# Optimization experiments

Measured on AMD Instinct MI355X. Metric: run time of the kernel, lower is better.

The kernel has to match this reference:

```python
import jax, jax.numpy as jnp
import numpy as np
from jax import lax

B, T, E, D, A, C, FILT = 32, 1600, 1024, 1024, 512, 10, 100
SCALING = 2.0


def setup_inputs() -> dict:
    key = jax.random.key(0)
    ks = jax.random.split(key, 14)
    enc_hs_pad = jax.random.normal(ks[0], (B, T, E), dtype=jnp.float32)
    # lengths in [T//2, T] so every row has valid positions
    enc_hs_len = jax.random.randint(ks[1], (B,), T // 2, T + 1, dtype=jnp.int32)
    dec_z = jax.random.normal(ks[2], (B, D), dtype=jnp.float32)
    # previous attention weights: uniform over valid frames, normalized
    valid = (jnp.arange(T)[None, :] < enc_hs_len[:, None]).astype(jnp.float32)
    raw = jax.random.uniform(ks[3], (B, T), dtype=jnp.float32) * valid
    att_prev = raw / jnp.sum(raw, axis=1, keepdims=True)
    att_h = 0.1 * jax.random.normal(ks[4], (B, A), dtype=jnp.float32)
    att_c = 0.1 * jax.random.normal(ks[5], (B, A), dtype=jnp.float32)
    W_enc = jax.random.normal(ks[6], (A, E), dtype=jnp.float32) / np.sqrt(E)
    b_enc = jax.random.normal(ks[7], (A,), dtype=jnp.float32) * 0.01
    W_dec = jax.random.normal(ks[8], (A, D), dtype=jnp.float32) / np.sqrt(D)
    conv_w = jax.random.normal(ks[9], (C, 1, 2 * FILT + 1), dtype=jnp.float32) / np.sqrt(2 * FILT + 1)
    W_ih = jax.random.normal(ks[10], (4 * A, C), dtype=jnp.float32) / np.sqrt(C)
    W_hh = jax.random.normal(ks[11], (4 * A, A), dtype=jnp.float32) / np.sqrt(A)
    W_g = jax.random.normal(ks[12], (A,), dtype=jnp.float32) / np.sqrt(A)
    b_g = jnp.zeros((1,), dtype=jnp.float32)
    return {"enc_hs_pad": enc_hs_pad, "enc_hs_len": enc_hs_len, "dec_z": dec_z,
            "att_prev": att_prev, "att_h": att_h, "att_c": att_c,
            "W_enc": W_enc, "b_enc": b_enc, "W_dec": W_dec, "conv_w": conv_w,
            "W_ih": W_ih, "W_hh": W_hh, "W_g": W_g, "b_g": b_g}


def reference(enc_hs_pad, enc_hs_len, dec_z, att_prev, att_h, att_c,
              W_enc, b_enc, W_dec, conv_w, W_ih, W_hh, W_g, b_g):
    t_len = enc_hs_pad.shape[1]
    filts = (conv_w.shape[-1] - 1) // 2

    # precompute encoder projection (B, T, A)
    pre_enc = jnp.einsum('bte,ae->bta', enc_hs_pad, W_enc) + b_enc

    # location conv on previous attention: (B,1,T) -> (B,C,T), relu, global max-pool over T
    att_conv = lax.conv_general_dilated(att_prev[:, None, :], conv_w,
                                        window_strides=(1,), padding=[(filts, filts)],
                                        dimension_numbers=('NCH', 'OIH', 'NCH'))
    att_feat = jnp.max(jax.nn.relu(att_conv), axis=-1)  # (B, C)

    # LSTMCell (no bias), pytorch gate order i, f, g, o
    gates = att_feat @ W_ih.T + att_h @ W_hh.T  # (B, 4A)
    i, f, g, o = jnp.split(gates, 4, axis=-1)
    c_new = jax.nn.sigmoid(f) * att_c + jax.nn.sigmoid(i) * jnp.tanh(g)
    h_new = jax.nn.sigmoid(o) * jnp.tanh(c_new)  # (B, A)

    dec_proj = dec_z @ W_dec.T  # (B, A)
    # scores (B, T)
    e = jnp.tanh(h_new[:, None, :] + pre_enc + dec_proj[:, None, :]) @ W_g + b_g

    mask = jnp.arange(t_len)[None, :] >= enc_hs_len[:, None]  # True = pad
    e = jnp.where(mask, jnp.finfo(e.dtype).min, e)
    w = jax.nn.softmax(SCALING * e, axis=1)  # (B, T)

    ctx = jnp.einsum('bt,bte->be', w, enc_hs_pad)  # (B, E)
    return ctx, w, h_new, c_new
```

## Files before the change

kernel.cpp:

```cpp
#include <hip/hip_runtime.h>
#include <hip/hip_bf16.h>

#define BB 32
#define TT 1600
#define EE 1024
#define AA 512
#define CC 10
#define KW 201

typedef __attribute__((ext_vector_type(8))) short short8;
typedef __attribute__((ext_vector_type(4))) float f32x4;

__device__ __forceinline__ float sigm(float x) { return 1.f / (1.f + expf(-x)); }

__device__ __forceinline__ unsigned int cvt2(float a, float b) {
    float2 f2; f2.x = a; f2.y = b;
    __hip_bfloat162 h = __float22bfloat162_rn(f2);
    unsigned int r;
    __builtin_memcpy(&r, &h, 4);
    return r;
}

__device__ __forceinline__ void gl_lds16(const void* g, void* l) {
    __builtin_amdgcn_global_load_lds(
        (const __attribute__((address_space(1))) unsigned int*)g,
        (__attribute__((address_space(3))) unsigned int*)l, 16, 0, 0);
}

#define AF_OFF   0
#define R_OFF    320
#define E_OFF    16704
#define WBF_OFF  67904

#define CTX_OFF 0
#define W_OFF   32768
#define H_OFF   83968
#define C_OFF   100352

__global__ void prep_kernel(const float* __restrict__ att_prev,
                            const float* __restrict__ conv_w,
                            const float* __restrict__ W_enc,
                            float* __restrict__ af,
                            unsigned short* __restrict__ Wbf) {
    int bx = blockIdx.x, tid = threadIdx.x;
    if (bx >= 320) {
        int i = (bx - 320) * 256 + tid;
        float4 v = reinterpret_cast<const float4*>(W_enc)[i];
        uint2 p;
        p.x = cvt2(v.x, v.y);
        p.y = cvt2(v.z, v.w);
        reinterpret_cast<uint2*>(Wbf)[i] = p;
        return;
    }
    int b = bx / 10, c = bx % 10;
    __shared__ float xs[1808];
    __shared__ float wsm[KW];
    __shared__ float red[256];
    const float* xp = att_prev + b * TT;
    for (int i = tid; i < 1808; i += 256) {
        int g = i - 100;
        xs[i] = (g >= 0 && g < TT) ? xp[g] : 0.f;
    }
    if (tid < KW) wsm[tid] = conv_w[c * KW + tid];
    __syncthreads();
    float mx = 0.f;
    #pragma unroll 1
    for (int sweep = 0; sweep < 2; ++sweep) {
        int t0 = sweep * 1024 + tid * 4;
        if (t0 >= TT) break;
        float a0 = xs[t0], a1 = xs[t0 + 1], a2 = xs[t0 + 2], a3 = xs[t0 + 3];
        float s0 = 0.f, s1 = 0.f, s2 = 0.f, s3 = 0.f;
        #pragma unroll 4
        for (int k = 0; k < KW; ++k) {
            float w = wsm[k];
            s0 += w * a0; s1 += w * a1; s2 += w * a2; s3 += w * a3;
            a0 = a1; a1 = a2; a2 = a3;
            a3 = xs[t0 + k + 4];
        }
        mx = fmaxf(mx, fmaxf(fmaxf(s0, s1), fmaxf(s2, s3)));
    }
    red[tid] = mx; __syncthreads();
    for (int s = 128; s > 0; s >>= 1) {
        if (tid < s) red[tid] = fmaxf(red[tid], red[tid + s]);
        __syncthreads();
    }
    if (tid == 0) af[b * CC + c] = red[0];
}

__global__ void gates_lstm_kernel(const float* __restrict__ af,
                                  const float* __restrict__ att_h,
                                  const float* __restrict__ dec_z,
                                  const float* __restrict__ att_c,
                                  const float* __restrict__ W_ih,
                                  const float* __restrict__ W_hh,
                                  const float* __restrict__ W_dec,
                                  float* __restrict__ out,
                                  float* __restrict__ r_ws) {
    __shared__ float gsm[8][32];
    __shared__ float dsm[8][32];
    int tid = threadIdx.x;
    int a0 = blockIdx.x * 2;
    int b = tid & 31;
    if (tid < 256) {
        int u = tid >> 5;
        int gate = u >> 1, ai = u & 1;
        int j = gate * 512 + a0 + ai;
        float s = 0.f;
        #pragma unroll
        for (int k = 0; k < 10; ++k) s += af[b * 10 + k] * W_ih[j * 10 + k];
        const float4* wr = reinterpret_cast<const float4*>(W_hh + (size_t)j * 512);
        const float4* hr = reinterpret_cast<const float4*>(att_h + b * 512);
        #pragma unroll 4
        for (int k = 0; k < 128; ++k) {
            float4 w = wr[k], h = hr[k];
            s += w.x * h.x + w.y * h.y + w.z * h.z + w.w * h.w;
        }
        gsm[u][b] = s;
    } else {
        int v = (tid - 256) >> 5;
        int ai = v & 1, q = v >> 1;
        int a = a0 + ai;
        const float4* wr = reinterpret_cast<const float4*>(W_dec + (size_t)a * 1024) + q * 64;
        const float4* zr = reinterpret_cast<const float4*>(dec_z + (size_t)b * 1024) + q * 64;
        float s = 0.f;
        #pragma unroll 4
        for (int k = 0; k < 64; ++k) {
            float4 w = wr[k], z = zr[k];
            s += w.x * z.x + w.y * z.y + w.z * z.z + w.w * z.w;
        }
        dsm[v][b] = s;
    }
    __syncthreads();
    if (tid < 64) {
        int ai = tid >> 5;
        int a = a0 + ai;
        float ig = gsm[ai][b], fg = gsm[2 + ai][b], gg = gsm[4 + ai][b], og = gsm[6 + ai][b];
        float cn = sigm(fg) * att_c[b * 512 + a] + sigm(ig) * tanhf(gg);
        float hn = sigm(og) * tanhf(cn);
        out[H_OFF + b * 512 + a] = hn;
        out[C_OFF + b * 512 + a] = cn;
        float dec = dsm[ai][b] + dsm[2 + ai][b] + dsm[4 + ai][b] + dsm[6 + ai][b];
        r_ws[b * 512 + a] = hn + dec;
    }
}

__global__ void __launch_bounds__(1024, 4)
score_gemm_kernel(const float* __restrict__ enc,
                  const unsigned short* __restrict__ Wbf,
                  const float* __restrict__ b_enc,
                  const float* __restrict__ r_ws,
                  const float* __restrict__ W_g,
                  float* __restrict__ e_ws) {
    __shared__ __align__(16) short Bs[3][16384];
    __shared__ __align__(16) char  AsB[3][16384];
    __shared__ float e_part[8][128];

    int tid = threadIdx.x;
    int lane = tid & 63, wv = tid >> 6;
    int wm = wv >> 3, wn = wv & 7;
    int col = lane & 15, quad = lane >> 4;
    int m0 = blockIdx.x * 128;

    int agrp = tid >> 7;
    int P = tid & 127;
    int Lc = P ^ ((P >> 3) & 7);
    int as_ = Lc >> 1, asub = Lc & 1;
    int akoct = as_ >> 4, arowin = as_ & 15;
    const float* asrc = enc + (size_t)(m0 + agrp * 16 + arowin) * EE + akoct * 8 + asub * 4;

    int L0 = (quad * 16 + col) * 2;
    int L1 = L0 + 1;
    int p0 = (L0 ^ ((L0 >> 3) & 7)) * 16;
    int p1 = (L1 ^ ((L1 >> 3) & 7)) * 16;

    int bslot = tid & 63;
    int boct = bslot >> 4, brow = bslot & 15;
    const unsigned short* bsrc0 = Wbf + (size_t)((tid >> 6) * 16 + brow) * EE + boct * 8;
    const unsigned short* bsrc1 = Wbf + (size_t)(((tid >> 6) + 16) * 16 + brow) * EE + boct * 8;

    f32x4 acc[4][2][2];
    #pragma unroll
    for (int mt = 0; mt < 4; ++mt)
        #pragma unroll
        for (int h = 0; h < 2; ++h)
            #pragma unroll
            for (int nt = 0; nt < 2; ++nt)
                acc[mt][h][nt] = (f32x4){0.f, 0.f, 0.f, 0.f};

    gl_lds16(asrc,              &AsB[0][tid * 16]);
    gl_lds16(bsrc0,             &Bs[0][tid * 8]);
    gl_lds16(bsrc1,             &Bs[0][8192 + tid * 8]);
    gl_lds16(asrc + 32,         &AsB[1][tid * 16]);
    gl_lds16(bsrc0 + 32,        &Bs[1][tid * 8]);
    gl_lds16(bsrc1 + 32,        &Bs[1][8192 + tid * 8]);
    asm volatile("s_waitcnt vmcnt(3)" ::: "memory");
    __builtin_amdgcn_s_barrier();

#define SCORE_CHUNK(KC, RB, SB, STAGE, SYNC, WN)                                \
    {                                                                           \
        if (STAGE) {                                                            \
            gl_lds16(asrc + ((KC) + 2) * 32,  &AsB[SB][tid * 16]);              \
            gl_lds16(bsrc0 + ((KC) + 2) * 32, &Bs[SB][tid * 8]);                \
            gl_lds16(bsrc1 + ((KC) + 2) * 32, &Bs[SB][8192 + tid * 8]);         \
        }                                                                       \
        short8 af[4];                                                           \
        _Pragma("unroll")                                                       \
        for (int mt = 0; mt < 4; ++mt) {                                        \
            const char* ab = &AsB[RB][(wm * 4 + mt) * 2048];                    \
            float4 x = *reinterpret_cast<const float4*>(ab + p0);               \
            float4 y = *reinterpret_cast<const float4*>(ab + p1);               \
            union { short8 s; unsigned int u[4]; } cv;                          \
            cv.u[0] = cvt2(x.x, x.y); cv.u[1] = cvt2(x.z, x.w);                 \
            cv.u[2] = cvt2(y.x, y.y); cv.u[3] = cvt2(y.z, y.w);                 \
            af[mt] = cv.s;                                                      \
        }                                                                       \
        short8 bf[2][2];                                                        \
        _Pragma("unroll")                                                       \
        for (int h = 0; h < 2; ++h)                                             \
            _Pragma("unroll")                                                   \
            for (int nt = 0; nt < 2; ++nt)                                      \
                bf[h][nt] = *reinterpret_cast<const short8*>(                   \
                    &Bs[RB][(h * 16 + wn * 2 + nt) * 512 + (quad * 16 + col) * 8]); \
        __builtin_amdgcn_s_setprio(1);                                          \
        _Pragma("unroll")                                                       \
        for (int mt = 0; mt < 4; ++mt)                                          \
            _Pragma("unroll")                                                   \
            for (int h = 0; h < 2; ++h)                                         \
                _Pragma("unroll")                                               \
                for (int nt = 0; nt < 2; ++nt)                                  \
                    acc[mt][h][nt] = __builtin_amdgcn_mfma_f32_16x16x32_bf16(   \
                        af[mt], bf[h][nt], acc[mt][h][nt], 0, 0, 0);            \
        __builtin_amdgcn_s_setprio(0);                                          \
        if (SYNC) {                                                             \
            asm volatile("s_waitcnt vmcnt(" #WN ")" ::: "memory");              \
            __builtin_amdgcn_s_barrier();                                       \
        }                                                                       \
    }

    #pragma unroll 1
    for (int c = 0; c < 30; c += 3) {
        SCORE_CHUNK(c,     0, 2, 1, 1, 3)
        SCORE_CHUNK(c + 1, 1, 0, 1, 1, 3)
        SCORE_CHUNK(c + 2, 2, 1, 1, 1, 3)
    }
    SCORE_CHUNK(30, 0, 0, 0, 1, 0)
    SCORE_CHUNK(31, 1, 0, 0, 0, 0)
#undef SCORE_CHUNK

    float wg[2][2], bn_[2][2];
    #pragma unroll
    for (int h = 0; h < 2; ++h)
        #pragma unroll
        for (int nt = 0; nt < 2; ++nt) {
            int n = h * 256 + wn * 32 + nt * 16 + col;
            wg[h][nt] = W_g[n];
            bn_[h][nt] = b_enc[n];
        }
    #pragma unroll
    for (int mt = 0; mt < 4; ++mt) {
        int mg = m0 + wm * 64 + mt * 16;
        int bb = mg / TT;
        float rr[2][2];
        #pragma unroll
        for (int h = 0; h < 2; ++h)
            #pragma unroll
            for (int nt = 0; nt < 2; ++nt)
                rr[h][nt] = r_ws[bb * AA + h * 256 + wn * 32 + nt * 16 + col];
        #pragma unroll
        for (int reg = 0; reg < 4; ++reg) {
            float p = 0.f;
            #pragma unroll
            for (int h = 0; h < 2; ++h)
                #pragma unroll
                for (int nt = 0; nt < 2; ++nt)
                    p += wg[h][nt] * tanhf(acc[mt][h][nt][reg] + bn_[h][nt] + rr[h][nt]);
            p += __shfl_xor(p, 1);
            p += __shfl_xor(p, 2);
            p += __shfl_xor(p, 4);
            p += __shfl_xor(p, 8);
            if (col == 0) e_part[wn][wm * 64 + mt * 16 + quad * 4 + reg] = p;
        }
    }
    __syncthreads();
    if (tid < 128) {
        float s = 0.f;
        #pragma unroll
        for (int i = 0; i < 8; ++i) s += e_part[i][tid];
        e_ws[m0 + tid] = s;
    }
}

__global__ void ctx_softmax_kernel(const float* __restrict__ enc,
                                   const float* __restrict__ e_ws,
                                   const int* __restrict__ lens,
                                   float* __restrict__ w_out,
                                   float* __restrict__ ctx) {
    int b = blockIdx.x, ch = blockIdx.y;
    int tid = threadIdx.x;
    __shared__ float w_sm[1600];
    __shared__ float red[512];
    __shared__ float part[8][128];
    int len = lens[b];
    const float* e = e_ws + b * TT;
    float mx = -3.4e38f;
    for (int t = tid; t < len; t += 512) mx = fmaxf(mx, e[t]);
    red[tid] = mx; __syncthreads();
    for (int s = 256; s > 0; s >>= 1) {
        if (tid < s) red[tid] = fmaxf(red[tid], red[tid + s]);
        __syncthreads();
    }
    mx = red[0]; __syncthreads();
    float sum = 0.f;
    for (int t = tid; t < TT; t += 512) {
        float p = (t < len) ? expf(2.f * (e[t] - mx)) : 0.f;
        w_sm[t] = p; sum += p;
    }
    red[tid] = sum; __syncthreads();
    for (int s = 256; s > 0; s >>= 1) {
        if (tid < s) red[tid] += red[tid + s];
        __syncthreads();
    }
    float inv = 1.f / red[0];
    __syncthreads();
    for (int t = tid; t < TT; t += 512) {
        float wv = w_sm[t] * inv;
        w_sm[t] = wv;
        if (ch == 0) w_out[b * TT + t] = wv;
    }
    __syncthreads();
    int lane2 = tid & 63, w8 = tid >> 6;
    int tb = w8 * 200;
    const float* base = enc + (size_t)(b * TT + tb) * EE + ch * 128 + lane2 * 2;
    float cx = 0.f, cy = 0.f;
    #pragma unroll 1
    for (int i = 0; i < 200; i += 8) {
        #pragma unroll
        for (int j = 0; j < 8; ++j) {
            float2 v = *reinterpret_cast<const float2*>(base + (size_t)(i + j) * EE);
            float ww = w_sm[tb + i + j];
            cx += ww * v.x; cy += ww * v.y;
        }
    }
    part[w8][lane2 * 2] = cx;
    part[w8][lane2 * 2 + 1] = cy;
    __syncthreads();
    if (tid < 128) {
        float s = 0.f;
        #pragma unroll
        for (int i = 0; i < 8; ++i) s += part[i][tid];
        ctx[b * EE + ch * 128 + tid] = s;
    }
}

extern "C" void kernel_launch(void* const* d_in, const int* in_sizes, int n_in,
                              void* d_out, int out_size, void* d_ws, size_t ws_size,
                              hipStream_t stream) {
    const float* enc      = (const float*)d_in[0];
    const int*   lens     = (const int*)d_in[1];
    const float* dec_z    = (const float*)d_in[2];
    const float* att_prev = (const float*)d_in[3];
    const float* att_h    = (const float*)d_in[4];
    const float* att_c    = (const float*)d_in[5];
    const float* W_enc    = (const float*)d_in[6];
    const float* b_enc    = (const float*)d_in[7];
    const float* W_dec    = (const float*)d_in[8];
    const float* conv_w   = (const float*)d_in[9];
    const float* W_ih     = (const float*)d_in[10];
    const float* W_hh     = (const float*)d_in[11];
    const float* W_g      = (const float*)d_in[12];

    float* out = (float*)d_out;
    float* ws  = (float*)d_ws;
    float* af   = ws + AF_OFF;
    float* r_ws = ws + R_OFF;
    float* e_ws = ws + E_OFF;
    unsigned short* Wbf = (unsigned short*)(ws + WBF_OFF);

    prep_kernel<<<832, 256, 0, stream>>>(att_prev, conv_w, W_enc, af, Wbf);
    gates_lstm_kernel<<<256, 512, 0, stream>>>(af, att_h, dec_z, att_c,
                                               W_ih, W_hh, W_dec, out, r_ws);
    score_gemm_kernel<<<400, 1024, 0, stream>>>(enc, Wbf, b_enc, r_ws, W_g, e_ws);
    ctx_softmax_kernel<<<dim3(BB, 8), 512, 0, stream>>>(enc, e_ws, lens,
                                                        out + W_OFF, out + CTX_OFF);
}
```

Before: 481.6 us.

## Stage encoder tile as bf16 via registers, double-buffer LDS to shrink footprint

```diff
diff --git a/kernel.cpp b/kernel.cpp
--- a/kernel.cpp
+++ b/kernel.cpp
@@ -144,16 +144,15 @@
     }
 }
 
-__global__ void __launch_bounds__(1024, 4)
+__global__ void __launch_bounds__(1024, 8)
 score_gemm_kernel(const float* __restrict__ enc,
                   const unsigned short* __restrict__ Wbf,
                   const float* __restrict__ b_enc,
                   const float* __restrict__ r_ws,
                   const float* __restrict__ W_g,
                   float* __restrict__ e_ws) {
-    __shared__ __align__(16) short Bs[3][16384];
-    __shared__ __align__(16) char  AsB[3][16384];
-    __shared__ float e_part[8][128];
+    __shared__ __align__(16) short Bs[2][16384];
+    __shared__ __align__(16) short As[2][4096];
 
     int tid = threadIdx.x;
     int lane = tid & 63, wv = tid >> 6;
@@ -161,17 +160,9 @@
     int col = lane & 15, quad = lane >> 4;
     int m0 = blockIdx.x * 128;
 
-    int agrp = tid >> 7;
-    int P = tid & 127;
-    int Lc = P ^ ((P >> 3) & 7);
-    int as_ = Lc >> 1, asub = Lc & 1;
-    int akoct = as_ >> 4, arowin = as_ & 15;
-    const float* asrc = enc + (size_t)(m0 + agrp * 16 + arowin) * EE + akoct * 8 + asub * 4;
-
-    int L0 = (quad * 16 + col) * 2;
-    int L1 = L0 + 1;
-    int p0 = (L0 ^ ((L0 >> 3) & 7)) * 16;
-    int p1 = (L1 ^ ((L1 >> 3) & 7)) * 16;
+    int arow = tid >> 3, akq2 = tid & 7;
+    const float* asrc = enc + (size_t)(m0 + arow) * EE + akq2 * 4;
+    int adst = (arow >> 4) * 512 + ((akq2 >> 1) * 16 + (arow & 15)) * 8 + (akq2 & 1) * 4;
 
     int bslot = tid & 63;
     int boct = bslot >> 4, brow = bslot & 15;
@@ -187,40 +178,42 @@
             for (int nt = 0; nt < 2; ++nt)
                 acc[mt][h][nt] = (f32x4){0.f, 0.f, 0.f, 0.f};
 
-    gl_lds16(asrc,              &AsB[0][tid * 16]);
-    gl_lds16(bsrc0,             &Bs[0][tid * 8]);
-    gl_lds16(bsrc1,             &Bs[0][8192 + tid * 8]);
-    gl_lds16(asrc + 32,         &AsB[1][tid * 16]);
-    gl_lds16(bsrc0 + 32,        &Bs[1][tid * 8]);
-    gl_lds16(bsrc1 + 32,        &Bs[1][8192 + tid * 8]);
-    asm volatile("s_waitcnt vmcnt(3)" ::: "memory");
-    __builtin_amdgcn_s_barrier();
-
-#define SCORE_CHUNK(KC, RB, SB, STAGE, SYNC, WN)                                \
+    float4 av0, av1;
+    {
+        float4 a0v = *reinterpret_cast<const float4*>(asrc);
+        gl_lds16(bsrc0, &Bs[0][tid * 8]);
+        gl_lds16(bsrc1, &Bs[0][8192 + tid * 8]);
+        __builtin_amdgcn_sched_barrier(0);
+        av1 = *reinterpret_cast<const float4*>(asrc + 32);
+        __builtin_amdgcn_sched_barrier(0);
+        uint2 q; q.x = cvt2(a0v.x, a0v.y); q.y = cvt2(a0v.z, a0v.w);
+        *reinterpret_cast<uint2*>(&As[0][adst]) = q;
+        asm volatile("s_waitcnt vmcnt(1) lgkmcnt(0)" ::: "memory");
+        __builtin_amdgcn_s_barrier();
+    }
+
+#define SCORE_CHUNK(KC, AVC, AVI, STAGEB, PREFA, WR, SYNC, WN)                  \
     {                                                                           \
-        if (STAGE) {                                                            \
-            gl_lds16(asrc + ((KC) + 2) * 32,  &AsB[SB][tid * 16]);              \
-            gl_lds16(bsrc0 + ((KC) + 2) * 32, &Bs[SB][tid * 8]);                \
-            gl_lds16(bsrc1 + ((KC) + 2) * 32, &Bs[SB][8192 + tid * 8]);         \
+        if (STAGEB) {                                                           \
+            gl_lds16(bsrc0 + ((KC) + 1) * 32, &Bs[((KC) + 1) & 1][tid * 8]);    \
+            gl_lds16(bsrc1 + ((KC) + 1) * 32, &Bs[((KC) + 1) & 1][8192 + tid * 8]); \
         }                                                                       \
+        __builtin_amdgcn_sched_barrier(0);                                      \
+        if (PREFA)                                                              \
+            AVI = *reinterpret_cast<const float4*>(asrc + ((KC) + 2) * 32);     \
+        __builtin_amdgcn_sched_barrier(0);                                      \
         short8 af[4];                                                           \
         _Pragma("unroll")                                                       \
-        for (int mt = 0; mt < 4; ++mt) {                                        \
-            const char* ab = &AsB[RB][(wm * 4 + mt) * 2048];                    \
-            float4 x = *reinterpret_cast<const float4*>(ab + p0);               \
-            float4 y = *reinterpret_cast<const float4*>(ab + p1);               \
-            union { short8 s; unsigned int u[4]; } cv;                          \
-            cv.u[0] = cvt2(x.x, x.y); cv.u[1] = cvt2(x.z, x.w);                 \
-            cv.u[2] = cvt2(y.x, y.y); cv.u[3] = cvt2(y.z, y.w);                 \
-            af[mt] = cv.s;                                                      \
-        }                                                                       \
+        for (int mt = 0; mt < 4; ++mt)                                          \
+            af[mt] = *reinterpret_cast<const short8*>(                          \
+                &As[(KC) & 1][(wm * 4 + mt) * 512 + (quad * 16 + col) * 8]);    \
         short8 bf[2][2];                                                        \
         _Pragma("unroll")                                                       \
         for (int h = 0; h < 2; ++h)                                             \
             _Pragma("unroll")                                                   \
             for (int nt = 0; nt < 2; ++nt)                                      \
                 bf[h][nt] = *reinterpret_cast<const short8*>(                   \
-                    &Bs[RB][(h * 16 + wn * 2 + nt) * 512 + (quad * 16 + col) * 8]); \
+                    &Bs[(KC) & 1][(h * 16 + wn * 2 + nt) * 512 + (quad * 16 + col) * 8]); \
         __builtin_amdgcn_s_setprio(1);                                          \
         _Pragma("unroll")                                                       \
         for (int mt = 0; mt < 4; ++mt)                                          \
@@ -231,22 +224,26 @@
                     acc[mt][h][nt] = __builtin_amdgcn_mfma_f32_16x16x32_bf16(   \
                         af[mt], bf[h][nt], acc[mt][h][nt], 0, 0, 0);            \
         __builtin_amdgcn_s_setprio(0);                                          \
+        if (WR) {                                                               \
+            uint2 q; q.x = cvt2(AVC.x, AVC.y); q.y = cvt2(AVC.z, AVC.w);        \
+            *reinterpret_cast<uint2*>(&As[((KC) + 1) & 1][adst]) = q;           \
+        }                                                                       \
         if (SYNC) {                                                             \
-            asm volatile("s_waitcnt vmcnt(" #WN ")" ::: "memory");              \
+            asm volatile("s_waitcnt vmcnt(" #WN ") lgkmcnt(0)" ::: "memory");   \
             __builtin_amdgcn_s_barrier();                                       \
         }                                                                       \
     }
 
     #pragma unroll 1
-    for (int c = 0; c < 30; c += 3) {
-        SCORE_CHUNK(c,     0, 2, 1, 1, 3)
-        SCORE_CHUNK(c + 1, 1, 0, 1, 1, 3)
-        SCORE_CHUNK(c + 2, 2, 1, 1, 1, 3)
-    }
-    SCORE_CHUNK(30, 0, 0, 0, 1, 0)
-    SCORE_CHUNK(31, 1, 0, 0, 0, 0)
+    for (int c = 0; c < 30; c += 2) {
+        SCORE_CHUNK(c,     av1, av0, 1, 1, 1, 1, 1)
+        SCORE_CHUNK(c + 1, av0, av1, 1, 1, 1, 1, 1)
+    }
+    SCORE_CHUNK(30, av1, av0, 1, 0, 1, 1, 0)
+    SCORE_CHUNK(31, av0, av1, 0, 0, 0, 0, 0)
 #undef SCORE_CHUNK
 
+    float (*e_part)[128] = reinterpret_cast<float (*)[128]>(&As[0][0]);
     float wg[2][2], bn_[2][2];
     #pragma unroll
     for (int h = 0; h < 2; ++h)
```

Result: slower. 1.511 ms (+213.8%).
